# Kernel optimization log

Measured on AMD Instinct MI355X. Metric: run time of the kernel, lower is better.

## Reference

```python
import jax, jax.numpy as jnp
import numpy as np

NUM_HEADS = 16
EMBED_DIM = 1024
HEAD_DIM = EMBED_DIM // NUM_HEADS


def setup_inputs() -> dict:
    key = jax.random.key(0)
    k1, k2, k3, k4, k5 = jax.random.split(key, 5)
    b, s, e = 2, 2048, EMBED_DIM
    x = jax.random.normal(k1, (b, s, e), dtype=jnp.float32)
    # torch Linear: y = x @ W.T + b, W shape (out, in)
    w_qkv = jax.random.normal(k2, (3 * e, e), dtype=jnp.float32) * (1.0 / np.sqrt(e))
    b_qkv = jax.random.normal(k3, (3 * e,), dtype=jnp.float32) * 0.02
    w_out = jax.random.normal(k4, (e, e), dtype=jnp.float32) * (1.0 / np.sqrt(e))
    b_out = jax.random.normal(k5, (e,), dtype=jnp.float32) * 0.02
    return {"x": x, "w_qkv": w_qkv, "b_qkv": b_qkv, "w_out": w_out,
            "b_out": b_out, "causal_mask": 1}


def reference(x, w_qkv, b_qkv, w_out, b_out, causal_mask):
    b, s, e = x.shape
    h, d = NUM_HEADS, HEAD_DIM
    qkv = x @ w_qkv.T + b_qkv                      # (b, s, 3e)
    # rearrange 'b s (three h d) -> b h s d three' -> split as (3, h, d)
    qkv = qkv.reshape(b, s, 3, h, d)
    q = jnp.transpose(qkv[:, :, 0], (0, 2, 1, 3))  # (b, h, s, d)
    k = jnp.transpose(qkv[:, :, 1], (0, 2, 1, 3))
    v = jnp.transpose(qkv[:, :, 2], (0, 2, 1, 3))
    scores = jnp.einsum('bhqd,bhkd->bhqk', q, k)   # (b, h, s, s)
    if causal_mask:
        mask = jnp.triu(jnp.ones((s, s), dtype=bool), 1)
        scores = jnp.where(mask, -jnp.inf, scores)
    scores = scores / np.sqrt(d).astype(np.float32)
    probs = jax.nn.softmax(scores, axis=-1)
    out = jnp.einsum('bhqk,bhkd->bhqd', probs, v)  # (b, h, s, d)
    out = jnp.transpose(out, (0, 2, 1, 3)).reshape(b, s, e)
    return out @ w_out.T + b_out
```

## Files before the change

### kernel.cpp

```cpp
#include <hip/hip_runtime.h>
#include <hip/hip_bf16.h>
#include <stdint.h>

static constexpr int S  = 2048;
static constexpr int NH = 16;
static constexpr int HD = 64;
static constexpr int E  = 1024;
static constexpr int BB = 2;
static constexpr int MR = BB * S;

typedef __attribute__((ext_vector_type(8))) short bf16x8;
typedef __attribute__((ext_vector_type(4))) float f32x4;
typedef __attribute__((ext_vector_type(16))) float f32x16;

__device__ __forceinline__ unsigned short f2bf(float f) {
  union { float f; unsigned u; } v; v.f = f;
  unsigned r = v.u + 0x7fffu + ((v.u >> 16) & 1u);
  return (unsigned short)(r >> 16);
}

__device__ __forceinline__ unsigned cvt_pk_bf16(float lo, float hi) {
  unsigned r;
  asm("v_cvt_pk_bf16_f32 %0, %1, %2" : "=v"(r) : "v"(lo), "v"(hi));
  return r;
}

__device__ __forceinline__ f32x4 mfma16(bf16x8 a, bf16x8 b, f32x4 c) {
  return __builtin_amdgcn_mfma_f32_16x16x32_bf16(a, b, c, 0, 0, 0);
}
__device__ __forceinline__ f32x16 mfma32(bf16x8 a, bf16x8 b, f32x16 c) {
  return __builtin_amdgcn_mfma_f32_32x32x16_bf16(a, b, c, 0, 0, 0);
}

__device__ __forceinline__ void gload_lds16(const void* g, void* l) {
  __builtin_amdgcn_global_load_lds(
      (const __attribute__((address_space(1))) uint32_t*)(uintptr_t)g,
      (__attribute__((address_space(3))) uint32_t*)(uintptr_t)l,
      16, 0, 0);
}

__global__ __launch_bounds__(256) void convert_bf16(
    const float* __restrict__ in, unsigned short* __restrict__ out, int n4) {
  int i = blockIdx.x * blockDim.x + threadIdx.x;
  const int stride = gridDim.x * blockDim.x;
  for (; i < n4; i += stride) {
    float4 v = ((const float4*)in)[i];
    ushort4 o;
    o.x = f2bf(v.x); o.y = f2bf(v.y); o.z = f2bf(v.z); o.w = f2bf(v.w);
    ((ushort4*)out)[i] = o;
  }
}

template <int EPI>
__global__ __launch_bounds__(256) void gemm_bt(
    const unsigned short* __restrict__ A, const unsigned short* __restrict__ W,
    const float* __restrict__ bias,
    void* __restrict__ o0, void* __restrict__ o1, void* __restrict__ o2,
    int M, int N, int K) {
  __shared__ __align__(16) unsigned short As[128 * 32];
  __shared__ __align__(16) unsigned short Bs[128 * 32];
  const int tid  = threadIdx.x;
  const int lane = tid & 63;
  const int wid  = tid >> 6;
  const int wm   = wid >> 1;
  const int wn   = wid & 1;
  const int g    = lane >> 4;
  const int lq   = lane & 15;
  const int row0 = blockIdx.y * 128;
  const int col0 = blockIdx.x * 128;
  const int srow = lane >> 2;
  const int sseg = (lane & 3) * 8;

  f32x4 acc[4][4] = {};

  for (int k0 = 0; k0 < K; k0 += 32) {
    __syncthreads();
#pragma unroll
    for (int cc = 0; cc < 2; ++cc) {
      const int c = wid + cc * 4;
      gload_lds16(A + (size_t)(row0 + c * 16 + srow) * K + k0 + sseg,
                  (char*)As + c * 1024);
      gload_lds16(W + (size_t)(col0 + c * 16 + srow) * K + k0 + sseg,
                  (char*)Bs + c * 1024);
    }
    __syncthreads();
    bf16x8 af[4], bfr[4];
#pragma unroll
    for (int m = 0; m < 4; ++m)
      af[m] = *(const bf16x8*)(As + (wm * 64 + m * 16 + lq) * 32 + g * 8);
#pragma unroll
    for (int n = 0; n < 4; ++n)
      bfr[n] = *(const bf16x8*)(Bs + (wn * 64 + n * 16 + lq) * 32 + g * 8);
#pragma unroll
    for (int m = 0; m < 4; ++m)
#pragma unroll
      for (int n = 0; n < 4; ++n)
        acc[m][n] = mfma16(af[m], bfr[n], acc[m][n]);
  }

  if (EPI == 0) {
    unsigned short* Qb = (unsigned short*)o0;
    unsigned short* Kb = (unsigned short*)o1;
    unsigned short* Vt = (unsigned short*)o2;
    const float qsc = 0.125f * 1.44269504f;
#pragma unroll
    for (int m = 0; m < 4; ++m) {
      const int rbase = row0 + wm * 64 + m * 16 + g * 4;
#pragma unroll
      for (int n = 0; n < 4; ++n) {
        const int col = col0 + wn * 64 + n * 16 + lq;
        const float bi = bias[col];
        const int three = col >> 10;
        const int rem = col & 1023;
        const int h = rem >> 6, d = rem & 63;
#pragma unroll
        for (int r = 0; r < 4; ++r) {
          const int row = rbase + r;
          const int bb = row >> 11, ss = row & 2047;
          float val = acc[m][n][r] + bi;
          if (three == 0) val *= qsc;
          const unsigned short bv = f2bf(val);
          if (three == 0)
            Qb[(((size_t)(bb * NH + h)) * S + ss) * HD + d] = bv;
          else if (three == 1)
            Kb[(((size_t)(bb * NH + h)) * S + ss) * HD + d] = bv;
          else
            Vt[(((size_t)(bb * NH + h)) * HD + d) * S + ss] = bv;
        }
      }
    }
  } else {
    float* Out = (float*)o0;
#pragma unroll
    for (int m = 0; m < 4; ++m) {
      const int rbase = row0 + wm * 64 + m * 16 + g * 4;
#pragma unroll
      for (int n = 0; n < 4; ++n) {
        const int col = col0 + wn * 64 + n * 16 + lq;
        const float bi = bias[col];
#pragma unroll
        for (int r = 0; r < 4; ++r)
          Out[(size_t)(rbase + r) * N + col] = acc[m][n][r] + bi;
      }
    }
  }
}

__global__ __launch_bounds__(128) void attn_fwd3(
    const unsigned short* __restrict__ Qb, const unsigned short* __restrict__ Kb,
    const unsigned short* __restrict__ Vt, unsigned short* __restrict__ Ao,
    const int* __restrict__ causal_p) {
  __shared__ __align__(16) unsigned short Ks[2][64 * 64];
  __shared__ __align__(16) unsigned short Vs[2][64 * 64];

  const int tid = threadIdx.x, lane = tid & 63, wid = tid >> 6;
  const int cq = lane & 31;
  const int hi = lane >> 5;
  const int id = blockIdx.x;
  const int swz = (id & 7) * 128 + (id >> 3);
  const int bh = swz >> 5;
  const int qt = 31 - (swz & 31);
  const int causal = *causal_p;
  const size_t base  = (size_t)bh * S * HD;
  const size_t vbase = (size_t)bh * HD * S;
  const int qw = qt * 64 + wid * 32;

  bf16x8 qf[4];
#pragma unroll
  for (int f = 0; f < 4; ++f)
    qf[f] = *(const bf16x8*)(Qb + base + (size_t)(qw + cq) * HD + f * 16 + hi * 8);

  float mM = -1e30f, lS = 0.f;
  f32x16 o0 = {}, o1 = {};

  const int r8 = lane >> 3;
  const int ssl = ((lane & 7) ^ r8) * 8;
  const int nkt = causal ? (qt + 1) : (S / 64);

#define STAGE(bufi, kt)                                                        \
  {                                                                            \
    _Pragma("unroll")                                                          \
    for (int i = 0; i < 4; ++i) {                                              \
      const int c = wid * 4 + i;                                               \
      gload_lds16(Kb + base + (size_t)((kt) * 64 + c * 8 + r8) * HD + ssl,     \
                  (char*)Ks[bufi] + c * 1024);                                 \
      gload_lds16(Vt + vbase + (size_t)(c * 8 + r8) * S + (kt) * 64 + ssl,     \
                  (char*)Vs[bufi] + c * 1024);                                 \
    }                                                                          \
  }

  STAGE(0, 0)
  int buf = 0;

  for (int kt = 0; kt < nkt; ++kt) {
    asm volatile("s_waitcnt vmcnt(0)" ::: "memory");
    __builtin_amdgcn_s_barrier();
    if (kt + 1 < nkt) STAGE(buf ^ 1, kt + 1)

    const char* Kp = (const char*)Ks[buf];
    const char* Vp = (const char*)Vs[buf];
    const int swb = (cq & 7) << 4;

    f32x16 sc0 = {}, sc1 = {};
    __builtin_amdgcn_s_setprio(1);
#pragma unroll
    for (int df = 0; df < 4; ++df) {
      const int colb = (df * 32 + hi * 16) ^ swb;
      bf16x8 k0 = *(const bf16x8*)(Kp + cq * 128 + colb);
      bf16x8 k1 = *(const bf16x8*)(Kp + (32 + cq) * 128 + colb);
      sc0 = mfma32(k0, qf[df], sc0);
      sc1 = mfma32(k1, qf[df], sc1);
    }
    __builtin_amdgcn_s_setprio(0);

    if (causal && kt == nkt - 1) {
      const int q = qw + cq;
      const int kb = kt * 64 + 4 * hi;
#pragma unroll
      for (int r = 0; r < 16; ++r) {
        const int kl = (r & 3) + 8 * (r >> 2);
        if (kb + kl > q)      sc0[r] = -1e30f;
        if (kb + 32 + kl > q) sc1[r] = -1e30f;
      }
    }

    float m0 = fmaxf(sc0[0], sc1[0]), m1 = fmaxf(sc0[1], sc1[1]);
    float m2 = fmaxf(sc0[2], sc1[2]), m3 = fmaxf(sc0[3], sc1[3]);
#pragma unroll
    for (int r = 4; r < 16; r += 4) {
      m0 = fmaxf(m0, fmaxf(sc0[r],     sc1[r]));
      m1 = fmaxf(m1, fmaxf(sc0[r + 1], sc1[r + 1]));
      m2 = fmaxf(m2, fmaxf(sc0[r + 2], sc1[r + 2]));
      m3 = fmaxf(m3, fmaxf(sc0[r + 3], sc1[r + 3]));
    }
    float mx = fmaxf(fmaxf(m0, m1), fmaxf(m2, m3));
    mx = fmaxf(mx, __shfl_xor(mx, 32));

    if (__any(mx > mM + 8.0f)) {
      const float mnew = fmaxf(mM, mx);
      const float al = exp2f(mM - mnew);
      mM = mnew;
      lS *= al; o0 *= al; o1 *= al;
    }

    float r0 = 0.f, r1 = 0.f, r2 = 0.f, r3 = 0.f;
#pragma unroll
    for (int r = 0; r < 16; r += 4) {
      sc0[r]     = exp2f(sc0[r]     - mM); sc1[r]     = exp2f(sc1[r]     - mM);
      sc0[r + 1] = exp2f(sc0[r + 1] - mM); sc1[r + 1] = exp2f(sc1[r + 1] - mM);
      sc0[r + 2] = exp2f(sc0[r + 2] - mM); sc1[r + 2] = exp2f(sc1[r + 2] - mM);
      sc0[r + 3] = exp2f(sc0[r + 3] - mM); sc1[r + 3] = exp2f(sc1[r + 3] - mM);
      r0 += sc0[r]     + sc1[r];
      r1 += sc0[r + 1] + sc1[r + 1];
      r2 += sc0[r + 2] + sc1[r + 2];
      r3 += sc0[r + 3] + sc1[r + 3];
    }
    float rs = (r0 + r1) + (r2 + r3);
    rs += __shfl_xor(rs, 32);
    lS += rs;

    unsigned w[16];
#pragma unroll
    for (int i = 0; i < 8; ++i) {
      w[i]     = cvt_pk_bf16(sc0[2 * i], sc0[2 * i + 1]);
      w[i + 8] = cvt_pk_bf16(sc1[2 * i], sc1[2 * i + 1]);
    }

#pragma unroll
    for (int m = 0; m < 4; ++m) {
      const unsigned a = w[4 * m], b = w[4 * m + 1], c = w[4 * m + 2], d = w[4 * m + 3];
      const unsigned ra = __shfl_xor((int)(hi ? a : c), 32);
      const unsigned rb = __shfl_xor((int)(hi ? b : d), 32);
      union { unsigned u[4]; bf16x8 v; } pf;
      pf.u[0] = hi ? ra : a;
      pf.u[1] = hi ? rb : b;
      pf.u[2] = hi ? c : ra;
      pf.u[3] = hi ? d : rb;
      const int colb = (m * 32 + hi * 16) ^ swb;
      bf16x8 v0 = *(const bf16x8*)(Vp + cq * 128 + colb);
      bf16x8 v1 = *(const bf16x8*)(Vp + (32 + cq) * 128 + colb);
      __builtin_amdgcn_s_setprio(1);
      o0 = mfma32(v0, pf.v, o0);
      o1 = mfma32(v1, pf.v, o1);
      __builtin_amdgcn_s_setprio(0);
    }
    buf ^= 1;
  }
#undef STAGE

  const int bb2 = bh >> 4, hh = bh & 15;
  unsigned short* orow = Ao + (((size_t)bb2 * S + (qw + cq)) * NH + hh) * HD;
  const float inv = 1.0f / lS;
#pragma unroll
  for (int i = 0; i < 4; ++i) {
    ushort4 u0, u1;
    u0.x = f2bf(o0[4 * i + 0] * inv); u0.y = f2bf(o0[4 * i + 1] * inv);
    u0.z = f2bf(o0[4 * i + 2] * inv); u0.w = f2bf(o0[4 * i + 3] * inv);
    u1.x = f2bf(o1[4 * i + 0] * inv); u1.y = f2bf(o1[4 * i + 1] * inv);
    u1.z = f2bf(o1[4 * i + 2] * inv); u1.w = f2bf(o1[4 * i + 3] * inv);
    *(ushort4*)(orow + i * 8 + 4 * hi) = u0;
    *(ushort4*)(orow + 32 + i * 8 + 4 * hi) = u1;
  }
}

extern "C" void kernel_launch(void* const* d_in, const int* in_sizes, int n_in,
                              void* d_out, int out_size, void* d_ws, size_t ws_size,
                              hipStream_t stream) {
  const float* x     = (const float*)d_in[0];
  const float* w_qkv = (const float*)d_in[1];
  const float* b_qkv = (const float*)d_in[2];
  const float* w_out = (const float*)d_in[3];
  const float* b_out = (const float*)d_in[4];
  const int*   causal = (const int*)d_in[5];

  char* ws = (char*)d_ws;
  unsigned short* xb    = (unsigned short*)(ws);
  unsigned short* wqkvb = (unsigned short*)(ws + 8388608);
  unsigned short* wob   = (unsigned short*)(ws + 14680064);
  unsigned short* Qb    = (unsigned short*)(ws + 16777216);
  unsigned short* Kb    = (unsigned short*)(ws + 25165824);
  unsigned short* Vtb   = (unsigned short*)(ws + 33554432);
  unsigned short* attnb = (unsigned short*)(ws + 41943040);

  convert_bf16<<<1024, 256, 0, stream>>>(x, xb, (BB * S * E) / 4);
  convert_bf16<<<1024, 256, 0, stream>>>(w_qkv, wqkvb, (3 * E * E) / 4);
  convert_bf16<<<512, 256, 0, stream>>>(w_out, wob, (E * E) / 4);

  gemm_bt<0><<<dim3(3 * E / 128, MR / 128), 256, 0, stream>>>(
      xb, wqkvb, b_qkv, Qb, Kb, Vtb, MR, 3 * E, E);

  attn_fwd3<<<1024, 128, 0, stream>>>(Qb, Kb, Vtb, attnb, causal);

  gemm_bt<1><<<dim3(E / 128, MR / 128), 256, 0, stream>>>(
      attnb, wob, b_out, d_out, nullptr, nullptr, MR, E, E);
}
```

Before: 259.5 us.

## Drop LDS staging in attention and load K/V fragments straight from global

The attention kernel no longer double-buffers K and V tiles through shared memory with barriers. Each wave now reads its MFMA K and V fragments directly from global memory, relying on L1/L2 caching. The block-to-tile mapping is simplified to spread heads across consecutive blocks, launch bounds now ask for 4 blocks per CU, and the bf16 packing is done per m-step. This removes LDS traffic and barrier stalls, but each wave issues its own uncoalesced global loads and gives up latency hiding from prefetch.

```diff
diff --git a/kernel.cpp b/kernel.cpp
--- a/kernel.cpp
+++ b/kernel.cpp
@@ -146,24 +146,21 @@
   }
 }
 
-__global__ __launch_bounds__(128) void attn_fwd3(
+__global__ __launch_bounds__(128, 4) void attn_fwd5(
     const unsigned short* __restrict__ Qb, const unsigned short* __restrict__ Kb,
     const unsigned short* __restrict__ Vt, unsigned short* __restrict__ Ao,
     const int* __restrict__ causal_p) {
-  __shared__ __align__(16) unsigned short Ks[2][64 * 64];
-  __shared__ __align__(16) unsigned short Vs[2][64 * 64];
-
   const int tid = threadIdx.x, lane = tid & 63, wid = tid >> 6;
   const int cq = lane & 31;
   const int hi = lane >> 5;
   const int id = blockIdx.x;
-  const int swz = (id & 7) * 128 + (id >> 3);
-  const int bh = swz >> 5;
-  const int qt = 31 - (swz & 31);
+  const int bh = id & 31;
+  const int ap = 31 - (id >> 5);
+  const int c  = ap * 2 + wid;
   const int causal = *causal_p;
   const size_t base  = (size_t)bh * S * HD;
   const size_t vbase = (size_t)bh * HD * S;
-  const int qw = qt * 64 + wid * 32;
+  const int qw = c * 32;
 
   bf16x8 qf[4];
 #pragma unroll
@@ -173,45 +170,33 @@
   float mM = -1e30f, lS = 0.f;
   f32x16 o0 = {}, o1 = {};
 
-  const int r8 = lane >> 3;
-  const int ssl = ((lane & 7) ^ r8) * 8;
-  const int nkt = causal ? (qt + 1) : (S / 64);
-
-#define STAGE(bufi, kt)                                                        \
-  {                                                                            \
-    _Pragma("unroll")                                                          \
-    for (int i = 0; i < 4; ++i) {                                              \
-      const int c = wid * 4 + i;                                               \
-      gload_lds16(Kb + base + (size_t)((kt) * 64 + c * 8 + r8) * HD + ssl,     \
-                  (char*)Ks[bufi] + c * 1024);                                 \
-      gload_lds16(Vt + vbase + (size_t)(c * 8 + r8) * S + (kt) * 64 + ssl,     \
-                  (char*)Vs[bufi] + c * 1024);                                 \
-    }                                                                          \
-  }
-
-  STAGE(0, 0)
-  int buf = 0;
+  const int nkt = causal ? (c / 2 + 1) : (S / 64);
 
   for (int kt = 0; kt < nkt; ++kt) {
-    asm volatile("s_waitcnt vmcnt(0)" ::: "memory");
-    __builtin_amdgcn_s_barrier();
-    if (kt + 1 < nkt) STAGE(buf ^ 1, kt + 1)
-
-    const char* Kp = (const char*)Ks[buf];
-    const char* Vp = (const char*)Vs[buf];
-    const int swb = (cq & 7) << 4;
+    const unsigned short* Kt = Kb + base + (size_t)(kt * 64) * HD;
+    bf16x8 k0[4], k1[4];
+#pragma unroll
+    for (int df = 0; df < 4; ++df) {
+      k0[df] = *(const bf16x8*)(Kt + (size_t)cq * HD + df * 16 + hi * 8);
+      k1[df] = *(const bf16x8*)(Kt + (size_t)(cq + 32) * HD + df * 16 + hi * 8);
+    }
 
     f32x16 sc0 = {}, sc1 = {};
     __builtin_amdgcn_s_setprio(1);
 #pragma unroll
     for (int df = 0; df < 4; ++df) {
-      const int colb = (df * 32 + hi * 16) ^ swb;
-      bf16x8 k0 = *(const bf16x8*)(Kp + cq * 128 + colb);
-      bf16x8 k1 = *(const bf16x8*)(Kp + (32 + cq) * 128 + colb);
-      sc0 = mfma32(k0, qf[df], sc0);
-      sc1 = mfma32(k1, qf[df], sc1);
+      sc0 = mfma32(k0[df], qf[df], sc0);
+      sc1 = mfma32(k1[df], qf[df], sc1);
     }
     __builtin_amdgcn_s_setprio(0);
+
+    const unsigned short* Vp = Vt + vbase + kt * 64;
+    bf16x8 v0[4], v1[4];
+#pragma unroll
+    for (int m = 0; m < 4; ++m) {
+      v0[m] = *(const bf16x8*)(Vp + (size_t)cq * S + m * 16 + hi * 8);
+      v1[m] = *(const bf16x8*)(Vp + (size_t)(cq + 32) * S + m * 16 + hi * 8);
+    }
 
     if (causal && kt == nkt - 1) {
       const int q = qw + cq;
@@ -259,34 +244,35 @@
     rs += __shfl_xor(rs, 32);
     lS += rs;
 
-    unsigned w[16];
-#pragma unroll
-    for (int i = 0; i < 8; ++i) {
-      w[i]     = cvt_pk_bf16(sc0[2 * i], sc0[2 * i + 1]);
-      w[i + 8] = cvt_pk_bf16(sc1[2 * i], sc1[2 * i + 1]);
-    }
-
 #pragma unroll
     for (int m = 0; m < 4; ++m) {
-      const unsigned a = w[4 * m], b = w[4 * m + 1], c = w[4 * m + 2], d = w[4 * m + 3];
-      const unsigned ra = __shfl_xor((int)(hi ? a : c), 32);
+      unsigned a, b, cc2, d;
+      if (m < 2) {
+        const int off = (m & 1) * 8;
+        a   = cvt_pk_bf16(sc0[off + 0], sc0[off + 1]);
+        b   = cvt_pk_bf16(sc0[off + 2], sc0[off + 3]);
+        cc2 = cvt_pk_bf16(sc0[off + 4], sc0[off + 5]);
+        d   = cvt_pk_bf16(sc0[off + 6], sc0[off + 7]);
+      } else {
+        const int off = (m & 1) * 8;
+        a   = cvt_pk_bf16(sc1[off + 0], sc1[off + 1]);
+        b   = cvt_pk_bf16(sc1[off + 2], sc1[off + 3]);
+        cc2 = cvt_pk_bf16(sc1[off + 4], sc1[off + 5]);
+        d   = cvt_pk_bf16(sc1[off + 6], sc1[off + 7]);
+      }
+      const unsigned ra = __shfl_xor((int)(hi ? a : cc2), 32);
       const unsigned rb = __shfl_xor((int)(hi ? b : d), 32);
       union { unsigned u[4]; bf16x8 v; } pf;
       pf.u[0] = hi ? ra : a;
       pf.u[1] = hi ? rb : b;
-      pf.u[2] = hi ? c : ra;
+      pf.u[2] = hi ? cc2 : ra;
       pf.u[3] = hi ? d : rb;
-      const int colb = (m * 32 + hi * 16) ^ swb;
-      bf16x8 v0 = *(const bf16x8*)(Vp + cq * 128 + colb);
-      bf16x8 v1 = *(const bf16x8*)(Vp + (32 + cq) * 128 + colb);
       __builtin_amdgcn_s_setprio(1);
-      o0 = mfma32(v0, pf.v, o0);
-      o1 = mfma32(v1, pf.v, o1);
+      o0 = mfma32(v0[m], pf.v, o0);
+      o1 = mfma32(v1[m], pf.v, o1);
       __builtin_amdgcn_s_setprio(0);
     }
-    buf ^= 1;
-  }
-#undef STAGE
+  }
 
   const int bb2 = bh >> 4, hh = bh & 15;
   unsigned short* orow = Ao + (((size_t)bb2 * S + (qw + cq)) * NH + hh) * HD;
@@ -329,7 +315,7 @@
   gemm_bt<0><<<dim3(3 * E / 128, MR / 128), 256, 0, stream>>>(
       xb, wqkvb, b_qkv, Qb, Kb, Vtb, MR, 3 * E, E);
 
-  attn_fwd3<<<1024, 128, 0, stream>>>(Qb, Kb, Vtb, attnb, causal);
+  attn_fwd5<<<1024, 128, 0, stream>>>(Qb, Kb, Vtb, attnb, causal);
 
   gemm_bt<1><<<dim3(E / 128, MR / 128), 256, 0, stream>>>(
       attnb, wob, b_out, d_out, nullptr, nullptr, MR, E, E);
```

Measured after the change: 281.7 us. 8.5% more time.
